# Kernel optimization log

Hardware: AMD Instinct MI355X
Metric: run time of the kernel (lower is better)

The kernel has to match this reference:

```python
import jax, jax.numpy as jnp
import numpy as np

S, B, E, F, H, NE, CAP = 2048, 4, 1024, 4096, 16, 8, 2048
LN_EPS = 1e-5


def _ln(x, s, b):
    m = jnp.mean(x, axis=-1, keepdims=True)
    v = jnp.mean((x - m) ** 2, axis=-1, keepdims=True)
    return (x - m) / jnp.sqrt(v + LN_EPS) * s + b


def _rope(x):
    # x: (S, B, E); rotary over full embed dim, half-split convention, base 10000
    d = x.shape[-1]
    inv = 1.0 / (10000.0 ** (jnp.arange(0, d // 2, dtype=jnp.float32) / (d // 2)))
    freqs = jnp.arange(x.shape[0], dtype=jnp.float32)[:, None] * inv[None, :]  # (S, d/2)
    cos = jnp.cos(freqs)[:, None, :]
    sin = jnp.sin(freqs)[:, None, :]
    x1, x2 = jnp.split(x, 2, axis=-1)
    return jnp.concatenate([x1 * cos - x2 * sin, x1 * sin + x2 * cos], axis=-1)


def setup_inputs():
    rng = jax.random.key(0)
    ks = jax.random.split(rng, 10)
    p = lambda k, sh: jax.random.normal(k, sh, jnp.float32) * 0.02
    return dict(
        query=jax.random.normal(ks[0], (S, B, E), jnp.float32),
        key=jax.random.normal(ks[1], (S, B, E), jnp.float32),
        value=jax.random.normal(ks[2], (S, B, E), jnp.float32),
        in_proj_w=p(ks[3], (3 * E, E)),
        in_proj_b=jnp.zeros((3 * E,), jnp.float32),
        out_proj_w=p(ks[4], (E, E)),
        out_proj_b=jnp.zeros((E,), jnp.float32),
        norm1_s=jnp.ones((E,), jnp.float32), norm1_b=jnp.zeros((E,), jnp.float32),
        norm2_s=jnp.ones((E,), jnp.float32), norm2_b=jnp.zeros((E,), jnp.float32),
        router_w=p(ks[5], (E, NE)),
        wi=p(ks[6], (NE, E, F)),
        wo=p(ks[7], (NE, F, E)),
    )


def reference(query, key, value, in_proj_w, in_proj_b, out_proj_w, out_proj_b,
              norm1_s, norm1_b, norm2_s, norm2_b, router_w, wi, wo):
    # pre-norm + rotary
    qn = _rope(_ln(query, norm1_s, norm1_b))
    kn = _rope(_ln(key, norm1_s, norm1_b))
    vn = _rope(_ln(value, norm1_s, norm1_b))

    # multi-head attention (seq-first layout, as in nn.MultiheadAttention default)
    hd = E // H
    qp = qn @ in_proj_w[:E].T + in_proj_b[:E]
    kp = kn @ in_proj_w[E:2 * E].T + in_proj_b[E:2 * E]
    vp = vn @ in_proj_w[2 * E:].T + in_proj_b[2 * E:]
    to_bhsd = lambda t: t.reshape(S, B, H, hd).transpose(1, 2, 0, 3)
    qh, kh, vh = to_bhsd(qp), to_bhsd(kp), to_bhsd(vp)
    scores = jnp.einsum('bhqd,bhkd->bhqk', qh, kh) / jnp.sqrt(jnp.float32(hd))
    attn = jax.nn.softmax(scores, axis=-1)
    ctx = jnp.einsum('bhqk,bhkd->bhqd', attn, vh)  # (B, H, S, hd)
    ctx = ctx.transpose(2, 0, 1, 3).reshape(S, B, E)
    attn_out = ctx @ out_proj_w.T + out_proj_b

    x = query + attn_out
    residual = x
    xn = _ln(x, norm2_s, norm2_b)

    # top-1 router with expert capacity (Switch-style)
    logits = xn.astype(jnp.float32) @ router_w  # (S, B, NE)
    top = jnp.argmax(logits, axis=-1)
    onehot = jax.nn.one_hot(top, NE, dtype=jnp.float32)  # (S, B, NE)
    flat = onehot.reshape(S * B, NE)
    pos = jnp.cumsum(flat, axis=0) * flat  # position within expert, 1-indexed
    keep = (pos <= CAP).astype(jnp.float32) * flat
    mask = jax.lax.stop_gradient(keep.reshape(S, B, NE))

    # expert FFNs: compute dense per expert, masked combine (same math as
    # boolean-index dispatch + zero-padded scatter + stacked masked sum)
    out = jnp.zeros_like(xn)
    for e in range(NE):
        h = jax.nn.gelu(xn @ wi[e], approximate=False) @ wo[e]
        out = out + h * mask[..., e:e + 1]

    return residual + out
```

## Files before the change

kernel.cpp:

```cpp
#include <hip/hip_runtime.h>
#include <math.h>

#define S_    2048
#define B_    4
#define E_    1024
#define F_    4096
#define H_    16
#define NE_   8
#define CAP_  2048
#define T_    (S_*B_)
#define HALF_ (E_/2)

typedef unsigned short u16;
typedef unsigned long long u64;
typedef __attribute__((ext_vector_type(8))) short bf16x8;
typedef __attribute__((ext_vector_type(4))) float f32x4;

__device__ __forceinline__ float bf2f(u16 u) {
  union { unsigned int i; float f; } v; v.i = ((unsigned int)u) << 16; return v.f;
}
__device__ __forceinline__ u16 f2bf(float f) {
  union { float f; unsigned int i; } v; v.f = f;
  unsigned int x = v.i;
  return (u16)((x + 0x7fffu + ((x >> 16) & 1u)) >> 16);
}
__device__ __forceinline__ void splitf(float v, u16& hi, u16& lo) {
  hi = f2bf(v);
  lo = f2bf(v - bf2f(hi));
}
__device__ __forceinline__ f32x4 mfma16(bf16x8 a, bf16x8 b, f32x4 c) {
  return __builtin_amdgcn_mfma_f32_16x16x32_bf16(a, b, c, 0, 0, 0);
}
__device__ __forceinline__ void glds16(const u16* g, u16* l) {
  __builtin_amdgcn_global_load_lds(
      (const __attribute__((address_space(1))) void*)g,
      (__attribute__((address_space(3))) void*)l, 16, 0, 0);
}

__global__ __launch_bounds__(256) void trig_kernel(float* __restrict__ cosT,
                                                   float* __restrict__ sinT) {
  int s = blockIdx.x;
  for (int j = threadIdx.x; j < HALF_; j += 256) {
    double inv = pow(10000.0, -(double)j / (double)HALF_);
    double fr = (double)s * inv;
    cosT[(size_t)s*HALF_ + j] = (float)cos(fr);
    sinT[(size_t)s*HALF_ + j] = (float)sin(fr);
  }
}

__global__ __launch_bounds__(256) void split_kernel(const float* __restrict__ src,
                                                    u16* __restrict__ hi, u16* __restrict__ lo, int n) {
  int i = blockIdx.x*256 + threadIdx.x;
  if (i < n) {
    float v = src[i];
    u16 h, l; splitf(v, h, l);
    hi[i] = h; lo[i] = l;
  }
}

__global__ __launch_bounds__(256) void transp_bf16_kernel(const float* __restrict__ src,
                                                          u16* __restrict__ dst, int R, int C) {
  int z = blockIdx.z;
  src += (size_t)z*R*C; dst += (size_t)z*R*C;
  __shared__ float tile[32][33];
  int r0 = blockIdx.y*32, c0 = blockIdx.x*32;
  int tr = threadIdx.x >> 5, tc = threadIdx.x & 31;
  for (int i = 0; i < 4; i++)
    tile[tr + i*8][tc] = src[(size_t)(r0 + tr + i*8)*C + c0 + tc];
  __syncthreads();
  for (int i = 0; i < 4; i++)
    dst[(size_t)(c0 + tr + i*8)*R + r0 + tc] = f2bf(tile[tc][tr + i*8]);
}

__global__ __launch_bounds__(256) void ln_rope_kernel(
    const float* __restrict__ in, const float* __restrict__ sw, const float* __restrict__ bw,
    const float* __restrict__ cosT, const float* __restrict__ sinT,
    u16* __restrict__ outh, u16* __restrict__ outl) {
  __shared__ float xb[E_];
  __shared__ double red[256];
  __shared__ double stats[2];
  int t = blockIdx.x;
  int s = t / B_;
  const float* row = in + (size_t)t * E_;
  int tid = threadIdx.x;
  double sum = 0.0;
  for (int k = 0; k < 4; k++) {
    int e = tid + k*256;
    float f = row[e];
    xb[e] = f;
    sum += (double)f;
  }
  red[tid] = sum; __syncthreads();
  for (int off = 128; off > 0; off >>= 1) {
    if (tid < off) red[tid] += red[tid+off];
    __syncthreads();
  }
  if (tid == 0) stats[0] = red[0] / (double)E_;
  __syncthreads();
  double m = stats[0];
  double sq = 0.0;
  for (int k = 0; k < 4; k++) {
    int e = tid + k*256;
    double d = (double)xb[e] - m;
    sq += d*d;
  }
  red[tid] = sq; __syncthreads();
  for (int off = 128; off > 0; off >>= 1) {
    if (tid < off) red[tid] += red[tid+off];
    __syncthreads();
  }
  if (tid == 0) stats[1] = 1.0 / sqrt(red[0] / (double)E_ + 1e-5);
  __syncthreads();
  float mf = (float)m, rs = (float)stats[1];
  for (int k = 0; k < 2; k++) {
    int j = tid + k*256;
    float n1 = (xb[j]        - mf)*rs*sw[j]        + bw[j];
    float n2 = (xb[j+HALF_]  - mf)*rs*sw[j+HALF_]  + bw[j+HALF_];
    float c  = cosT[(size_t)s*HALF_ + j];
    float sn = sinT[(size_t)s*HALF_ + j];
    float o1 = n1*c - n2*sn;
    float o2 = n1*sn + n2*c;
    u16 h, l;
    splitf(o1, h, l);
    outh[(size_t)t*E_ + j] = h; outl[(size_t)t*E_ + j] = l;
    splitf(o2, h, l);
    outh[(size_t)t*E_ + HALF_ + j] = h; outl[(size_t)t*E_ + HALF_ + j] = l;
  }
}

__global__ __launch_bounds__(256) void ln2_kernel(
    const float* __restrict__ in, const float* __restrict__ sw, const float* __restrict__ bw,
    float* __restrict__ out, u16* __restrict__ outb) {
  __shared__ float xb[E_];
  __shared__ double red[256];
  __shared__ double stats[2];
  int t = blockIdx.x;
  const float* row = in + (size_t)t * E_;
  int tid = threadIdx.x;
  double sum = 0.0;
  for (int k = 0; k < 4; k++) {
    int e = tid + k*256;
    float f = row[e];
    xb[e] = f;
    sum += (double)f;
  }
  red[tid] = sum; __syncthreads();
  for (int off = 128; off > 0; off >>= 1) {
    if (tid < off) red[tid] += red[tid+off];
    __syncthreads();
  }
  if (tid == 0) stats[0] = red[0] / (double)E_;
  __syncthreads();
  double m = stats[0];
  double sq = 0.0;
  for (int k = 0; k < 4; k++) {
    int e = tid + k*256;
    double d = (double)xb[e] - m;
    sq += d*d;
  }
  red[tid] = sq; __syncthreads();
  for (int off = 128; off > 0; off >>= 1) {
    if (tid < off) red[tid] += red[tid+off];
    __syncthreads();
  }
  if (tid == 0) stats[1] = 1.0 / sqrt(red[0] / (double)E_ + 1e-5);
  __syncthreads();
  float mf = (float)m, rs = (float)stats[1];
  for (int k = 0; k < 4; k++) {
    int e = tid + k*256;
    float v = (xb[e] - mf)*rs*sw[e] + bw[e];
    out[(size_t)t*E_ + e] = v;
    outb[(size_t)t*E_ + e] = f2bf(v);
  }
}

template<int MODE>
__global__ __launch_bounds__(256) void gemm_mfma(
    const u16* __restrict__ Ah, const u16* __restrict__ Al,
    const u16* __restrict__ Bh, const u16* __restrict__ Bl,
    const float* __restrict__ bias, const float* __restrict__ res,
    float* __restrict__ Cf, u16* __restrict__ Ch, u16* __restrict__ Cl,
    int M, int N, int K) {
  __shared__ u16 Ash[128][40];
  __shared__ u16 Bsh[128][40];
  __shared__ u16 Asl[128][40];
  __shared__ u16 Bsl[128][40];
  int tid = threadIdx.x;
  int m0 = blockIdx.y*128, n0 = blockIdx.x*128;
  if constexpr (MODE == 0) {
    int z = blockIdx.z;
    Ah += (size_t)z*M*K;  Al += (size_t)z*M*K;
    Bh += (size_t)z*N*K;  Bl += (size_t)z*N*K;
    bias += (size_t)z*N;
    Ch += (size_t)z*M*N;  Cl += (size_t)z*M*N;
  }
  int wave = tid>>6, lane = tid&63, quad = lane>>4, l16 = lane&15;
  int wm = (wave>>1)*64, wn = (wave&1)*64;
  f32x4 acc[4][4];
  for (int i = 0; i < 4; i++)
    for (int j = 0; j < 4; j++)
      acc[i][j] = f32x4{0.f, 0.f, 0.f, 0.f};
  for (int k0 = 0; k0 < K; k0 += 32) {
    for (int c = tid; c < 512; c += 256) {
      int r = c >> 2, k8 = (c & 3) * 8;
      *(int4*)&Ash[r][k8] = *(const int4*)(Ah + (size_t)(m0+r)*K + k0 + k8);
      *(int4*)&Asl[r][k8] = *(const int4*)(Al + (size_t)(m0+r)*K + k0 + k8);
      *(int4*)&Bsh[r][k8] = *(const int4*)(Bh + (size_t)(n0+r)*K + k0 + k8);
      *(int4*)&Bsl[r][k8] = *(const int4*)(Bl + (size_t)(n0+r)*K + k0 + k8);
    }
    __syncthreads();
    bf16x8 af[4], bf[4];
    bf16x8 afl[4], bfl[4];
#pragma unroll
    for (int t4 = 0; t4 < 4; t4++) {
      af[t4] = *(const bf16x8*)&Ash[wm + t4*16 + l16][quad*8];
      bf[t4] = *(const bf16x8*)&Bsh[wn + t4*16 + l16][quad*8];
      afl[t4] = *(const bf16x8*)&Asl[wm + t4*16 + l16][quad*8];
      bfl[t4] = *(const bf16x8*)&Bsl[wn + t4*16 + l16][quad*8];
    }
#pragma unroll
    for (int i = 0; i < 4; i++)
#pragma unroll
      for (int j = 0; j < 4; j++) {
        f32x4 a = acc[i][j];
        a = mfma16(af[i],  bf[j],  a);
        a = mfma16(af[i],  bfl[j], a);
        a = mfma16(afl[i], bf[j],  a);
        acc[i][j] = a;
      }
    __syncthreads();
  }
  for (int i = 0; i < 4; i++) {
    for (int j = 0; j < 4; j++) {
      for (int r = 0; r < 4; r++) {
        int rl  = wm + i*16 + quad*4 + r;
        int col = n0 + wn + j*16 + l16;
        float v = acc[i][j][r];
        if constexpr (MODE == 0) {
          v += bias[col];
          u16 hi, lo; splitf(v, hi, lo);
          size_t o = (size_t)(m0+rl)*N + col;
          Ch[o] = hi; Cl[o] = lo;
        } else {
          size_t o = (size_t)(m0+rl)*N + col;
          Cf[o] = v + bias[col] + res[o];
        }
      }
    }
  }
}

template<int MODE>
__global__ __launch_bounds__(256) void gemm_gather(
    const u16* __restrict__ A, const u16* __restrict__ B,
    const float* __restrict__ res,
    float* __restrict__ Cf, u16* __restrict__ Ch,
    int N, int K,
    const int* __restrict__ elist, const int* __restrict__ ecount) {
  __shared__ u16 As[2][128][32];
  __shared__ u16 Bs[2][128][32];
  __shared__ int toks[128];
  int tid = threadIdx.x;
  int m0 = blockIdx.y*128, n0 = blockIdx.x*128;
  int e = blockIdx.z;
  int cnt = ecount[e];
  if (m0 >= cnt) return;
  B += (size_t)e*N*K;
  const int* el = elist + e*CAP_;
  if (tid < 128) {
    int r = m0 + tid;
    toks[tid] = (r < cnt) ? el[r] : -1;
  }
  __syncthreads();
  int r0 = tid >> 2, ch0 = tid & 3;
  int r1 = r0 + 64;
  int s8 = (ch0 ^ (r0 & 3)) * 8;
  int tokA0 = toks[r0], tokA1 = toks[r1];
  const u16* gA0 = A + (size_t)(tokA0 >= 0 ? tokA0 : 0)*K + s8;
  const u16* gA1 = A + (size_t)(tokA1 >= 0 ? tokA1 : 0)*K + s8;
  const u16* gB0 = B + (size_t)(n0 + r0)*K + s8;
  const u16* gB1 = B + (size_t)(n0 + r1)*K + s8;
  u16* dA0 = &As[0][r0][ch0*8];
  u16* dA1 = &As[0][r1][ch0*8];
  u16* dB0 = &Bs[0][r0][ch0*8];
  u16* dB1 = &Bs[0][r1][ch0*8];
  int wave = tid>>6, lane = tid&63, quad = lane>>4, l16 = lane&15;
  int wm = (wave>>1)*64, wn = (wave&1)*64;
  int chA = (quad ^ (l16 & 3)) * 8;
  f32x4 acc[4][4];
  for (int i = 0; i < 4; i++)
    for (int j = 0; j < 4; j++)
      acc[i][j] = f32x4{0.f, 0.f, 0.f, 0.f};
  glds16(gA0, dA0); glds16(gA1, dA1);
  glds16(gB0, dB0); glds16(gB1, dB1);
  asm volatile("s_waitcnt vmcnt(0)" ::: "memory");
  __builtin_amdgcn_s_barrier();
  int cur = 0;
  for (int k0 = 0; k0 < K; k0 += 32) {
    int nxt = cur ^ 1;
    if (k0 + 32 < K) {
      int ko = k0 + 32;
      glds16(gA0 + ko, dA0 + nxt*4096); glds16(gA1 + ko, dA1 + nxt*4096);
      glds16(gB0 + ko, dB0 + nxt*4096); glds16(gB1 + ko, dB1 + nxt*4096);
    }
    const u16* aS = &As[cur][0][0];
    const u16* bS = &Bs[cur][0][0];
    bf16x8 af[4], bfr[4];
#pragma unroll
    for (int t4 = 0; t4 < 4; t4++) {
      af[t4]  = *(const bf16x8*)(aS + (wm + t4*16 + l16)*32 + chA);
      bfr[t4] = *(const bf16x8*)(bS + (wn + t4*16 + l16)*32 + chA);
    }
#pragma unroll
    for (int i = 0; i < 4; i++)
#pragma unroll
      for (int j = 0; j < 4; j++)
        acc[i][j] = mfma16(af[i], bfr[j], acc[i][j]);
    asm volatile("s_waitcnt vmcnt(0)" ::: "memory");
    __builtin_amdgcn_s_barrier();
    cur = nxt;
  }
  for (int i = 0; i < 4; i++) {
    for (int j = 0; j < 4; j++) {
      for (int r = 0; r < 4; r++) {
        int rl  = wm + i*16 + quad*4 + r;
        int col = n0 + wn + j*16 + l16;
        float v = acc[i][j][r];
        int tok = toks[rl];
        if (tok >= 0) {
          if constexpr (MODE == 2) {
            float g = 0.5f*v*(1.0f + erff(v*0.70710678118654752f));
            Ch[(size_t)tok*N + col] = f2bf(g);
          } else {
            size_t o = (size_t)tok*N + col;
            Cf[o] = v + res[o];
          }
        }
      }
    }
  }
}

__global__ __launch_bounds__(256) void attn_mfma_kernel(
    const u16* __restrict__ qh_, const u16* __restrict__ ql_,
    const u16* __restrict__ kh_, const u16* __restrict__ kl_,
    const u16* __restrict__ vh_, const u16* __restrict__ vl_,
    u16* __restrict__ ch_, u16* __restrict__ cl_) {
  __shared__ u16 Kh[64][72], Kl[64][72];
  __shared__ u16 Vth[64][72], Vtl[64][72];
  __shared__ u16 Ph[64][72], Pl[64][72];
  int bh = blockIdx.y;
  int b = bh >> 4, hh = bh & 15;
  int q0 = blockIdx.x * 64;
  int tid = threadIdx.x, wave = tid>>6, lane = tid&63, quad = lane>>4, l16 = lane&15;
  bf16x8 qfh[2], qfl[2];
  {
    int qrow = q0 + wave*16 + l16;
    size_t base = ((size_t)qrow*B_ + b)*E_ + hh*64;
    for (int st = 0; st < 2; st++) {
      qfh[st] = *(const bf16x8*)(qh_ + base + st*32 + quad*8);
      qfl[st] = *(const bf16x8*)(ql_ + base + st*32 + quad*8);
    }
  }
  float m_i[4], l_i[4];
  f32x4 acc[4];
  for (int r = 0; r < 4; r++) { m_i[r] = -INFINITY; l_i[r] = 0.f; }
  for (int d = 0; d < 4; d++) acc[d] = f32x4{0.f,0.f,0.f,0.f};
  for (int kt = 0; kt < S_/64; kt++) {
    __syncthreads();
    for (int c = tid; c < 512; c += 256) {
      int r = c >> 3, k8 = (c & 7) * 8;
      size_t gb = ((size_t)(kt*64 + r)*B_ + b)*E_ + hh*64 + k8;
      *(int4*)&Kh[r][k8] = *(const int4*)(kh_ + gb);
      *(int4*)&Kl[r][k8] = *(const int4*)(kl_ + gb);
      u16 tmp[8];
      *(int4*)tmp = *(const int4*)(vh_ + gb);
#pragma unroll
      for (int i = 0; i < 8; i++) Vth[k8+i][r] = tmp[i];
      *(int4*)tmp = *(const int4*)(vl_ + gb);
#pragma unroll
      for (int i = 0; i < 8; i++) Vtl[k8+i][r] = tmp[i];
    }
    __syncthreads();
    f32x4 sc[4];
#pragma unroll
    for (int ct = 0; ct < 4; ct++) {
      f32x4 s = f32x4{0.f,0.f,0.f,0.f};
#pragma unroll
      for (int st = 0; st < 2; st++) {
        bf16x8 kh = *(const bf16x8*)&Kh[ct*16 + l16][st*32 + quad*8];
        bf16x8 kl = *(const bf16x8*)&Kl[ct*16 + l16][st*32 + quad*8];
        s = mfma16(qfh[st], kh, s);
        s = mfma16(qfh[st], kl, s);
        s = mfma16(qfl[st], kh, s);
      }
      sc[ct] = s;
    }
#pragma unroll
    for (int ct = 0; ct < 4; ct++)
#pragma unroll
      for (int r = 0; r < 4; r++)
        sc[ct][r] *= 0.125f;
    float mx[4], alpha[4], rs[4];
#pragma unroll
    for (int r = 0; r < 4; r++)
      mx[r] = fmaxf(fmaxf(sc[0][r], sc[1][r]), fmaxf(sc[2][r], sc[3][r]));
#pragma unroll
    for (int off = 1; off < 16; off <<= 1)
#pragma unroll
      for (int r = 0; r < 4; r++)
        mx[r] = fmaxf(mx[r], __shfl_xor(mx[r], off, 64));
#pragma unroll
    for (int r = 0; r < 4; r++) {
      float mn = fmaxf(m_i[r], mx[r]);
      alpha[r] = expf(m_i[r] - mn);
      m_i[r] = mn;
      rs[r] = 0.f;
    }
#pragma unroll
    for (int ct = 0; ct < 4; ct++)
#pragma unroll
      for (int r = 0; r < 4; r++) {
        float p = expf(sc[ct][r] - m_i[r]);
        sc[ct][r] = p;
        rs[r] += p;
      }
#pragma unroll
    for (int off = 1; off < 16; off <<= 1)
#pragma unroll
      for (int r = 0; r < 4; r++)
        rs[r] += __shfl_xor(rs[r], off, 64);
#pragma unroll
    for (int r = 0; r < 4; r++)
      l_i[r] = l_i[r]*alpha[r] + rs[r];
#pragma unroll
    for (int ct = 0; ct < 4; ct++)
#pragma unroll
      for (int r = 0; r < 4; r++) {
        u16 hi, lo; splitf(sc[ct][r], hi, lo);
        int q = wave*16 + quad*4 + r;
        int k = ct*16 + l16;
        Ph[q][k] = hi; Pl[q][k] = lo;
      }
#pragma unroll
    for (int d = 0; d < 4; d++)
#pragma unroll
      for (int r = 0; r < 4; r++)
        acc[d][r] *= alpha[r];
    __syncthreads();
#pragma unroll
    for (int dt = 0; dt < 4; dt++) {
      f32x4 a = acc[dt];
#pragma unroll
      for (int st = 0; st < 2; st++) {
        bf16x8 ph = *(const bf16x8*)&Ph[wave*16 + l16][st*32 + quad*8];
        bf16x8 pl = *(const bf16x8*)&Pl[wave*16 + l16][st*32 + quad*8];
        bf16x8 vh = *(const bf16x8*)&Vth[dt*16 + l16][st*32 + quad*8];
        bf16x8 vl = *(const bf16x8*)&Vtl[dt*16 + l16][st*32 + quad*8];
        a = mfma16(ph, vh, a);
        a = mfma16(ph, vl, a);
        a = mfma16(pl, vh, a);
      }
      acc[dt] = a;
    }
  }
  for (int dt = 0; dt < 4; dt++) {
    for (int r = 0; r < 4; r++) {
      float v = acc[dt][r] / l_i[r];
      int q = q0 + wave*16 + quad*4 + r;
      size_t o = ((size_t)q*B_ + b)*E_ + hh*64 + dt*16 + l16;
      u16 hi, lo; splitf(v, hi, lo);
      ch_[o] = hi; cl_[o] = lo;
    }
  }
}

__global__ __launch_bounds__(256) void router_kernel(
    const float* __restrict__ xn, const float* __restrict__ rw, int* __restrict__ top) {
  __shared__ float lg[32][9];
  int t0 = blockIdx.x * 32;
  int tl = threadIdx.x >> 3;
  int n = threadIdx.x & 7;
  int t = t0 + tl;
  const float* xr = xn + (size_t)t * E_;
  double acc = 0.0;
  for (int e = 0; e < E_; e++) acc += (double)xr[e] * (double)rw[e*NE_ + n];
  lg[tl][n] = (float)acc;
  __syncthreads();
  if (n == 0) {
    float best = lg[tl][0]; int bi = 0;
    for (int i = 1; i < 8; i++) {
      float v = lg[tl][i];
      if (v > best) { best = v; bi = i; }
    }
    top[t] = bi;
  }
}

__global__ __launch_bounds__(256) void capacity_kernel(
    const int* __restrict__ top, int* __restrict__ elist, int* __restrict__ ecount) {
  __shared__ int tl[T_];
  __shared__ int cnts[256][NE_];
  int tid = threadIdx.x;
  for (int i = tid; i < T_; i += 256) tl[i] = top[i];
  __syncthreads();
  int c[NE_] = {};
  int base = tid * 32;
  for (int i = 0; i < 32; i++) c[tl[base+i]]++;
  for (int n = 0; n < NE_; n++) cnts[tid][n] = c[n];
  __syncthreads();
  if (tid < NE_) {
    int run = 0;
    for (int i = 0; i < 256; i++) {
      int v = cnts[i][tid];
      cnts[i][tid] = run;
      run += v;
    }
    ecount[tid] = min(run, CAP_);
  }
  __syncthreads();
  int pos[NE_];
  for (int n = 0; n < NE_; n++) pos[n] = cnts[tid][n];
  for (int i = 0; i < 32; i++) {
    int t = base + i;
    int e = tl[t];
    int p = pos[e]++;
    if (p < CAP_) elist[e*CAP_ + p] = t;
  }
}

__global__ __launch_bounds__(256) void fill_out_kernel(
    const float* __restrict__ x, float* __restrict__ out) {
  size_t i4 = ((size_t)blockIdx.x*256 + threadIdx.x) * 4;
  *(float4*)(out + i4) = *(const float4*)(x + i4);
}

extern "C" void kernel_launch(void* const* d_in, const int* in_sizes, int n_in,
                              void* d_out, int out_size, void* d_ws, size_t ws_size,
                              hipStream_t stream) {
  (void)in_sizes; (void)n_in; (void)out_size; (void)ws_size;
  const float* query      = (const float*)d_in[0];
  const float* key        = (const float*)d_in[1];
  const float* value      = (const float*)d_in[2];
  const float* in_proj_w  = (const float*)d_in[3];
  const float* in_proj_b  = (const float*)d_in[4];
  const float* out_proj_w = (const float*)d_in[5];
  const float* out_proj_b = (const float*)d_in[6];
  const float* norm1_s    = (const float*)d_in[7];
  const float* norm1_b    = (const float*)d_in[8];
  const float* norm2_s    = (const float*)d_in[9];
  const float* norm2_b    = (const float*)d_in[10];
  const float* router_w   = (const float*)d_in[11];
  const float* wi         = (const float*)d_in[12];
  const float* wo         = (const float*)d_in[13];
  float* out = (float*)d_out;

  char* wsb = (char*)d_ws;
  const size_t TE = (size_t)T_ * E_;
  u16* nh  = (u16*)(wsb + 0);
  u16* nl  = nh + 3*TE;
  u16* wit = (u16*)(wsb + 0);
  u16* wot = wit + (size_t)8*F_*E_;
  u16* pph  = (u16*)(wsb + 134217728ULL);
  u16* ppl  = pph + 3*TE;
  u16* hbuf = (u16*)(wsb + 134217728ULL);
  u16* xnb  = hbuf + (size_t)T_*F_;
  u16* ctxh = (u16*)(wsb + 234881024ULL);
  u16* ctxl = ctxh + TE;
  float* xn = (float*)(wsb + 234881024ULL);
  float* x  = (float*)(wsb + 268435456ULL);
  float* cosT = (float*)(wsb + 301989888ULL);
  float* sinT = cosT + (size_t)S_*HALF_;
  u16* iph = (u16*)(wsb + 310378496ULL);
  u16* ipl = iph + (size_t)3*E_*E_;
  u16* oph = ipl + (size_t)3*E_*E_;
  u16* opl = oph + (size_t)E_*E_;
  int* top    = (int*)(wsb + 327155712ULL);
  int* elist  = top + T_;
  int* ecount = elist + NE_*CAP_;

  trig_kernel<<<dim3(S_), dim3(256), 0, stream>>>(cosT, sinT);
  split_kernel<<<dim3((3*E_*E_)/256), dim3(256), 0, stream>>>(in_proj_w, iph, ipl, 3*E_*E_);
  split_kernel<<<dim3((E_*E_)/256), dim3(256), 0, stream>>>(out_proj_w, oph, opl, E_*E_);
  ln_rope_kernel<<<dim3(T_), dim3(256), 0, stream>>>(query, norm1_s, norm1_b, cosT, sinT, nh,        nl);
  ln_rope_kernel<<<dim3(T_), dim3(256), 0, stream>>>(key,   norm1_s, norm1_b, cosT, sinT, nh + TE,   nl + TE);
  ln_rope_kernel<<<dim3(T_), dim3(256), 0, stream>>>(value, norm1_s, norm1_b, cosT, sinT, nh + 2*TE, nl + 2*TE);
  gemm_mfma<0><<<dim3(E_/128, T_/128, 3), dim3(256), 0, stream>>>(
      nh, nl, iph, ipl, in_proj_b, nullptr, nullptr, pph, ppl,
      T_, E_, E_);
  transp_bf16_kernel<<<dim3(F_/32, E_/32, 8), dim3(256), 0, stream>>>(wi, wit, E_, F_);
  transp_bf16_kernel<<<dim3(E_/32, F_/32, 8), dim3(256), 0, stream>>>(wo, wot, F_, E_);
  attn_mfma_kernel<<<dim3(S_/64, B_*H_), dim3(256), 0, stream>>>(
      pph, ppl, pph + TE, ppl + TE, pph + 2*TE, ppl + 2*TE, ctxh, ctxl);
  gemm_mfma<1><<<dim3(E_/128, T_/128, 1), dim3(256), 0, stream>>>(
      ctxh, ctxl, oph, opl, out_proj_b, query, x, nullptr, nullptr,
      T_, E_, E_);
  ln2_kernel<<<dim3(T_), dim3(256), 0, stream>>>(x, norm2_s, norm2_b, xn, xnb);
  router_kernel<<<dim3(T_/32), dim3(256), 0, stream>>>(xn, router_w, top);
  capacity_kernel<<<dim3(1), dim3(256), 0, stream>>>(top, elist, ecount);
  fill_out_kernel<<<dim3(TE/1024), dim3(256), 0, stream>>>(x, out);
  gemm_gather<2><<<dim3(F_/128, CAP_/128, NE_), dim3(256), 0, stream>>>(
      xnb, wit, nullptr, nullptr, hbuf, F_, E_, elist, ecount);
  gemm_gather<3><<<dim3(E_/128, CAP_/128, NE_), dim3(256), 0, stream>>>(
      hbuf, wot, x, out, nullptr, E_, F_, elist, ecount);
}
```

Baseline: 1.798 ms.

## Pre-transpose V and register-prefetch next K/V tile in attention

A new kernel transposes the V projection into a per-head (d, s) layout ahead of time. The attention kernel can then stage V with 16-byte LDS stores instead of scalar transposed stores. The K and V loads for the next tile are issued into registers before the current tile's MFMAs, overlapping global latency with compute, and one barrier is dropped because each wave only reads its own P rows. LDS row padding shrinks from 72 to 68 elements, which may leave the 16-byte bf16x8 LDS reads misaligned and adds register pressure.

```diff
diff --git a/kernel.cpp b/kernel.cpp
--- a/kernel.cpp
+++ b/kernel.cpp
@@ -70,6 +70,28 @@
   __syncthreads();
   for (int i = 0; i < 4; i++)
     dst[(size_t)(c0 + tr + i*8)*R + r0 + tc] = f2bf(tile[tc][tr + i*8]);
+}
+
+__global__ __launch_bounds__(256) void vtransp_kernel(
+    const u16* __restrict__ vh, const u16* __restrict__ vl,
+    u16* __restrict__ dh, u16* __restrict__ dl) {
+  __shared__ u16 tile[32][34];
+  int s0 = blockIdx.x * 32;
+  int d0 = blockIdx.y * 32;
+  int bh = blockIdx.z;
+  int b = bh >> 4, h = bh & 15;
+  int tr = threadIdx.x >> 5, tc = threadIdx.x & 31;
+#pragma unroll
+  for (int comp = 0; comp < 2; comp++) {
+    const u16* src = comp ? vl : vh;
+    u16* dst = comp ? dl : dh;
+    for (int i = 0; i < 4; i++)
+      tile[tr + i*8][tc] = src[((size_t)(s0 + tr + i*8)*B_ + b)*E_ + h*64 + d0 + tc];
+    __syncthreads();
+    for (int i = 0; i < 4; i++)
+      dst[((size_t)bh*64 + d0 + tr + i*8)*S_ + s0 + tc] = tile[tc][tr + i*8];
+    __syncthreads();
+  }
 }
 
 __global__ __launch_bounds__(256) void ln_rope_kernel(
@@ -344,11 +366,11 @@
 __global__ __launch_bounds__(256) void attn_mfma_kernel(
     const u16* __restrict__ qh_, const u16* __restrict__ ql_,
     const u16* __restrict__ kh_, const u16* __restrict__ kl_,
-    const u16* __restrict__ vh_, const u16* __restrict__ vl_,
+    const u16* __restrict__ vth_, const u16* __restrict__ vtl_,
     u16* __restrict__ ch_, u16* __restrict__ cl_) {
-  __shared__ u16 Kh[64][72], Kl[64][72];
-  __shared__ u16 Vth[64][72], Vtl[64][72];
-  __shared__ u16 Ph[64][72], Pl[64][72];
+  __shared__ u16 Kh[64][68], Kl[64][68];
+  __shared__ u16 Vth[64][68], Vtl[64][68];
+  __shared__ u16 Ph[64][68], Pl[64][68];
   int bh = blockIdx.y;
   int b = bh >> 4, hh = bh & 15;
   int q0 = blockIdx.x * 64;
@@ -362,26 +384,32 @@
       qfl[st] = *(const bf16x8*)(ql_ + base + st*32 + quad*8);
     }
   }
+  int sr0 = tid >> 3, sk = (tid & 7) * 8;
+  int sr1 = sr0 + 32;
+  int4 rKh0, rKl0, rVh0, rVl0, rKh1, rKl1, rVh1, rVl1;
+  auto issue = [&](int kt) {
+    size_t gb0 = ((size_t)(kt*64 + sr0)*B_ + b)*E_ + hh*64 + sk;
+    size_t gb1 = ((size_t)(kt*64 + sr1)*B_ + b)*E_ + hh*64 + sk;
+    size_t gv0 = ((size_t)bh*64 + sr0)*S_ + kt*64 + sk;
+    size_t gv1 = ((size_t)bh*64 + sr1)*S_ + kt*64 + sk;
+    rKh0 = *(const int4*)(kh_ + gb0);  rKl0 = *(const int4*)(kl_ + gb0);
+    rKh1 = *(const int4*)(kh_ + gb1);  rKl1 = *(const int4*)(kl_ + gb1);
+    rVh0 = *(const int4*)(vth_ + gv0); rVl0 = *(const int4*)(vtl_ + gv0);
+    rVh1 = *(const int4*)(vth_ + gv1); rVl1 = *(const int4*)(vtl_ + gv1);
+  };
   float m_i[4], l_i[4];
   f32x4 acc[4];
   for (int r = 0; r < 4; r++) { m_i[r] = -INFINITY; l_i[r] = 0.f; }
   for (int d = 0; d < 4; d++) acc[d] = f32x4{0.f,0.f,0.f,0.f};
+  issue(0);
   for (int kt = 0; kt < S_/64; kt++) {
     __syncthreads();
-    for (int c = tid; c < 512; c += 256) {
-      int r = c >> 3, k8 = (c & 7) * 8;
-      size_t gb = ((size_t)(kt*64 + r)*B_ + b)*E_ + hh*64 + k8;
-      *(int4*)&Kh[r][k8] = *(const int4*)(kh_ + gb);
-      *(int4*)&Kl[r][k8] = *(const int4*)(kl_ + gb);
-      u16 tmp[8];
-      *(int4*)tmp = *(const int4*)(vh_ + gb);
-#pragma unroll
-      for (int i = 0; i < 8; i++) Vth[k8+i][r] = tmp[i];
-      *(int4*)tmp = *(const int4*)(vl_ + gb);
-#pragma unroll
-      for (int i = 0; i < 8; i++) Vtl[k8+i][r] = tmp[i];
-    }
-    __syncthreads();
+    *(int4*)&Kh[sr0][sk] = rKh0;  *(int4*)&Kl[sr0][sk] = rKl0;
+    *(int4*)&Kh[sr1][sk] = rKh1;  *(int4*)&Kl[sr1][sk] = rKl1;
+    *(int4*)&Vth[sr0][sk] = rVh0; *(int4*)&Vtl[sr0][sk] = rVl0;
+    *(int4*)&Vth[sr1][sk] = rVh1; *(int4*)&Vtl[sr1][sk] = rVl1;
+    __syncthreads();
+    if (kt + 1 < S_/64) issue(kt + 1);
     f32x4 sc[4];
 #pragma unroll
     for (int ct = 0; ct < 4; ct++) {
@@ -447,7 +475,6 @@
 #pragma unroll
       for (int r = 0; r < 4; r++)
         acc[d][r] *= alpha[r];
-    __syncthreads();
 #pragma unroll
     for (int dt = 0; dt < 4; dt++) {
       f32x4 a = acc[dt];
@@ -568,6 +595,8 @@
   u16* ctxh = (u16*)(wsb + 234881024ULL);
   u16* ctxl = ctxh + TE;
   float* xn = (float*)(wsb + 234881024ULL);
+  u16* vth = (u16*)(wsb + 268435456ULL);
+  u16* vtl = vth + TE;
   float* x  = (float*)(wsb + 268435456ULL);
   float* cosT = (float*)(wsb + 301989888ULL);
   float* sinT = cosT + (size_t)S_*HALF_;
@@ -588,10 +617,12 @@
   gemm_mfma<0><<<dim3(E_/128, T_/128, 3), dim3(256), 0, stream>>>(
       nh, nl, iph, ipl, in_proj_b, nullptr, nullptr, pph, ppl,
       T_, E_, E_);
+  vtransp_kernel<<<dim3(S_/32, 2, B_*H_), dim3(256), 0, stream>>>(
+      pph + 2*TE, ppl + 2*TE, vth, vtl);
   transp_bf16_kernel<<<dim3(F_/32, E_/32, 8), dim3(256), 0, stream>>>(wi, wit, E_, F_);
   transp_bf16_kernel<<<dim3(E_/32, F_/32, 8), dim3(256), 0, stream>>>(wo, wot, F_, E_);
   attn_mfma_kernel<<<dim3(S_/64, B_*H_), dim3(256), 0, stream>>>(
-      pph, ppl, pph + TE, ppl + TE, pph + 2*TE, ppl + 2*TE, ctxh, ctxl);
+      pph, ppl, pph + TE, ppl + TE, vth, vtl, ctxh, ctxl);
   gemm_mfma<1><<<dim3(E_/128, T_/128, 1), dim3(256), 0, stream>>>(
       ctxh, ctxl, oph, opl, out_proj_b, query, x, nullptr, nullptr,
       T_, E_, E_);
```

After: 1.595 ms. -11.3%, faster.
